# Optimization experiments

Measured on AMD Instinct MI355X. Metric: run time of the kernel, lower is better.

## Reference

```python
import jax, jax.numpy as jnp
import numpy as np

DIM = 256
STATE = 128
RANK = 64
BATCH = 16
H = 64
W = 64
BLOCK = 64
LN_EPS = 1e-5


def _linear(z, w, b):
    # torch nn.Linear: z @ w.T + b, w: [out, in]
    return jnp.matmul(z, w.T) + b


def _depthwise_conv1d(y, conv_w, conv_b):
    # y: [B, L, D] -> torch Conv1d(D, D, k=7, pad=3, groups=D)
    lhs = jnp.transpose(y, (0, 2, 1))  # [B, D, L]
    out = jax.lax.conv_general_dilated(
        lhs, conv_w, window_strides=(1,), padding=[(3, 3)],
        feature_group_count=STATE,
        dimension_numbers=("NCH", "OIH", "NCH"))
    out = out + conv_b[None, :, None]
    return jnp.transpose(out, (0, 2, 1))  # [B, L, D]


def _scan_parallel(seq, in_proj_w, in_proj_b, U, V, B_w, B_b, out_w, out_b,
                   conv_w, conv_b):
    # seq: [B, L, C]; L > PARALLEL_THRESHOLD path of the torch module
    Bn, L, _ = seq.shape
    x = _linear(seq, in_proj_w, in_proj_b)   # [B, L, D]
    bx = _linear(x, B_w, B_b)                # [B, L, D]
    n_blocks = (L + BLOCK - 1) // BLOCK
    pad_len = n_blocks * BLOCK - L
    if pad_len > 0:
        bx = jnp.pad(bx, ((0, 0), (0, pad_len), (0, 0)))
    # [B, n_blocks, BLOCK, D] -> scan over time axis BLOCK
    bx_blocks = bx.reshape(Bn, n_blocks, BLOCK, STATE)
    bx_t = jnp.transpose(bx_blocks, (2, 0, 1, 3))  # [BLOCK, B, n_blocks, D]

    def step(h, xt):
        # h: [B, n_blocks, D]; low-rank transition h @ V @ U^T + Bx
        h = jnp.matmul(jnp.matmul(h, V), U.T) + xt
        return h, h

    h0 = jnp.zeros((Bn, n_blocks, STATE), dtype=seq.dtype)
    _, ys = jax.lax.scan(step, h0, bx_t)           # [BLOCK, B, n_blocks, D]
    y_flat = jnp.transpose(ys, (1, 2, 0, 3)).reshape(Bn, n_blocks * BLOCK, STATE)
    y_flat = y_flat + _depthwise_conv1d(y_flat, conv_w, conv_b)
    if pad_len > 0:
        y_flat = y_flat[:, :L, :]
    return _linear(y_flat, out_w, out_b)           # [B, L, C]


def _layer_norm(z, g, b):
    mu = jnp.mean(z, axis=-1, keepdims=True)
    var = jnp.var(z, axis=-1, keepdims=True)
    return (z - mu) * jax.lax.rsqrt(var + LN_EPS) * g + b


def setup_inputs() -> dict:
    key = jax.random.key(0)
    ks = jax.random.split(key, 16)
    s = 0.02
    return {
        "x": jax.random.normal(ks[0], (BATCH, DIM, H, W), dtype=jnp.float32),
        "in_proj_w": jax.random.normal(ks[1], (STATE, DIM)) * s,
        "in_proj_b": jnp.zeros((STATE,), jnp.float32),
        "U": jax.random.normal(ks[2], (STATE, RANK)) * s,
        "V": jax.random.normal(ks[3], (STATE, RANK)) * s,
        "B_w": jax.random.normal(ks[4], (STATE, STATE)) * s,
        "B_b": jnp.zeros((STATE,), jnp.float32),
        "out_w": jax.random.normal(ks[5], (DIM, STATE)) * s,
        "out_b": jnp.zeros((DIM,), jnp.float32),
        "gate_w": jax.random.normal(ks[6], (DIM, DIM)) * s,
        "gate_b": jnp.zeros((DIM,), jnp.float32),
        "norm_g": jnp.ones((DIM,), jnp.float32),
        "norm_b": jnp.zeros((DIM,), jnp.float32),
        "conv_w": jax.random.normal(ks[7], (STATE, 1, 7)) * s,
        "conv_b": jnp.zeros((STATE,), jnp.float32),
    }


def reference(x, in_proj_w, in_proj_b, U, V, B_w, B_b, out_w, out_b,
              gate_w, gate_b, norm_g, norm_b, conv_w, conv_b):
    Bn, C, h, w = x.shape
    seq_lr = jnp.transpose(x, (0, 2, 3, 1)).reshape(Bn, h * w, C)
    seq_rl = seq_lr[:, ::-1, :]
    scan = lambda s: _scan_parallel(s, in_proj_w, in_proj_b, U, V, B_w, B_b,
                                    out_w, out_b, conv_w, conv_b)
    y_lr = scan(seq_lr)
    y_rl = scan(seq_rl)[:, ::-1, :]
    y = 0.5 * (y_lr + y_rl)
    gate = jax.nn.sigmoid(_linear(seq_lr, gate_w, gate_b))
    y = gate * y
    y = _layer_norm(y + seq_lr, norm_g, norm_b)
    y = jnp.transpose(y.reshape(Bn, h, w, C), (0, 3, 1, 2))
    state_seq = _linear(seq_lr, in_proj_w, in_proj_b)
    return y, state_seq
```

## Files before the change

### kernel.cpp

```cpp
#include <hip/hip_runtime.h>
#include <hip/hip_bf16.h>

#define DIMC 256
#define STATE 128
#define RANK 64
#define NBATCH 16
#define LSEQ 4096
#define NROWS (NBATCH*LSEQ)
#define LN_EPS 1e-5f
#define XSTR 264
#define X1STR 136

typedef __attribute__((ext_vector_type(8))) short frag8;
typedef __attribute__((ext_vector_type(4))) float f32x4;

union AFrag { __hip_bfloat16 h[8]; frag8 f; };
union Pack4 { __hip_bfloat16 h[4]; uint2 u; };
union Pack8 { __hip_bfloat16 h[8]; uint4 u; };

__device__ inline void gload_lds16(const void* g, void* l) {
    __builtin_amdgcn_global_load_lds((const __attribute__((address_space(1))) void*)g,
                                     (__attribute__((address_space(3))) void*)l, 16, 0, 0);
}

__device__ inline void stage_wslice(const __hip_bfloat16* __restrict__ W, int Krow, int k0,
                                    __hip_bfloat16* dst, int t, int nrows) {
    const int lane = t & 63, w = t >> 6;
    const int rounds = nrows >> 6;
    for (int j = 0; j < rounds; ++j) {
        int base = (w*rounds + j) << 10;
        int X = base + lane*16;
        int r = X >> 6;
        int cg = (X >> 4) & 3;
        const __hip_bfloat16* src = W + (size_t)r*Krow + k0 + ((cg ^ ((r>>1)&3)) << 3);
        gload_lds16(src, (char*)dst + base);
    }
}
__device__ inline frag8 ld_wfrag(const __hip_bfloat16* buf, int row, int q) {
    return *(const frag8*)((const char*)buf + (row<<6) + ((q ^ ((row>>1)&3))<<4));
}

__global__ __launch_bounds__(128) void a_kernel(const float* __restrict__ U, const float* __restrict__ V,
                                                __hip_bfloat16* __restrict__ At) {
    int i = blockIdx.x, j = threadIdx.x;
    float s = 0.f;
    #pragma unroll
    for (int r = 0; r < RANK; ++r) s += V[i*RANK + r] * U[j*RANK + r];
    At[j*STATE + i] = __float2bfloat16(s);
}

__global__ __launch_bounds__(256) void prep_weights(const float* __restrict__ in_w, const float* __restrict__ B_w,
                                                    const float* __restrict__ gate_w, const float* __restrict__ out_w,
                                                    __hip_bfloat16* __restrict__ in_wb, __hip_bfloat16* __restrict__ B_wb,
                                                    __hip_bfloat16* __restrict__ gate_wb, __hip_bfloat16* __restrict__ out_wb) {
    int idx = blockIdx.x*256 + threadIdx.x;
    int which = blockIdx.y;
    if (which == 0) { if (idx < STATE*DIMC)  in_wb[idx]   = __float2bfloat16(in_w[idx]); }
    else if (which == 1) { if (idx < STATE*STATE) B_wb[idx] = __float2bfloat16(B_w[idx]); }
    else if (which == 2) { if (idx < DIMC*DIMC)  gate_wb[idx] = __float2bfloat16(gate_w[idx]); }
    else { if (idx < DIMC*STATE) out_wb[idx] = __float2bfloat16(out_w[idx]); }
}

template<int LROWS>
__device__ inline void stage_x_tile(const float* __restrict__ xb, int l0,
                                    __hip_bfloat16* __restrict__ xs, int t) {
    constexpr int NP = LROWS/4;
    #pragma unroll
    for (int p = 0; p < NP; ++p) {
        int cin = (t>>2) + (p&3)*64;
        int lq  = (t&3) + (p>>2)*4;
        float4 v = *(const float4*)(xb + (size_t)cin*LSEQ + l0 + lq*4);
        int lb = lq*4;
        xs[(size_t)(lb+0)*XSTR + (cin ^ 0 )] = __float2bfloat16(v.x);
        xs[(size_t)(lb+1)*XSTR + (cin ^ 8 )] = __float2bfloat16(v.y);
        xs[(size_t)(lb+2)*XSTR + (cin ^ 16)] = __float2bfloat16(v.z);
        xs[(size_t)(lb+3)*XSTR + (cin ^ 24)] = __float2bfloat16(v.w);
    }
}
__device__ inline frag8 ld_xfrag(const __hip_bfloat16* __restrict__ xs, int row, int k) {
    return *(const frag8*)(xs + (size_t)row*XSTR + (k ^ ((row&3)<<3)));
}

__global__ __launch_bounds__(256) void gemm_inB(const float* __restrict__ x,
                                                const __hip_bfloat16* __restrict__ in_wb, const float* __restrict__ in_b,
                                                const __hip_bfloat16* __restrict__ B_wb, const float* __restrict__ B_b,
                                                float* __restrict__ state_out, float* __restrict__ bx) {
    __shared__ __hip_bfloat16 xs[64*XSTR];
    __shared__ __hip_bfloat16 wsl[2][4096];
    __hip_bfloat16* x1s = xs;
    const int t = threadIdx.x;
    const int lane = t & 63;
    const int c = lane & 15, q = lane >> 4;
    const int wm = t >> 6;
    const int r0 = blockIdx.x * 64;
    const int b = r0 >> 12, l0 = r0 & 4095;

    stage_x_tile<64>(x + (size_t)b*DIMC*LSEQ, l0, xs, t);
    stage_wslice(in_wb, DIMC, 0, wsl[0], t, STATE);
    __syncthreads();

    f32x4 acc[8] = {};
    #pragma unroll
    for (int i = 0; i < 8; ++i) {
        if (i < 7) stage_wslice(in_wb, DIMC, (i+1)*32, wsl[(i+1)&1], t, STATE);
        frag8 af = ld_xfrag(xs, wm*16 + c, i*32 + q*8);
        #pragma unroll
        for (int nt = 0; nt < 8; ++nt) {
            frag8 bf = ld_wfrag(wsl[i&1], nt*16 + c, q);
            acc[nt] = __builtin_amdgcn_mfma_f32_16x16x32_bf16(af, bf, acc[nt], 0, 0, 0);
        }
        __syncthreads();
    }

    stage_wslice(B_wb, STATE, 0, wsl[0], t, STATE);

    #pragma unroll
    for (int nt = 0; nt < 8; ++nt) {
        float bb = in_b[nt*16 + c];
        int col = nt*16 + c;
        #pragma unroll
        for (int r = 0; r < 4; ++r) {
            int row = wm*16 + q*4 + r;
            float v = acc[nt][r] + bb;
            state_out[(size_t)(r0 + row)*STATE + col] = v;
            x1s[(size_t)row*X1STR + (col ^ ((row&3)<<3))] = __float2bfloat16(v);
        }
    }
    __syncthreads();

    f32x4 acc2[8] = {};
    #pragma unroll
    for (int i = 0; i < 4; ++i) {
        if (i < 3) stage_wslice(B_wb, STATE, (i+1)*32, wsl[(i+1)&1], t, STATE);
        int row = wm*16 + c;
        frag8 af = *(const frag8*)(x1s + (size_t)row*X1STR + (((i*32) + q*8) ^ ((row&3)<<3)));
        #pragma unroll
        for (int nt = 0; nt < 8; ++nt) {
            frag8 bf = ld_wfrag(wsl[i&1], nt*16 + c, q);
            acc2[nt] = __builtin_amdgcn_mfma_f32_16x16x32_bf16(af, bf, acc2[nt], 0, 0, 0);
        }
        __syncthreads();
    }
    const int orow = r0 + wm*16 + q*4;
    #pragma unroll
    for (int nt = 0; nt < 8; ++nt) {
        float bb = B_b[nt*16 + c];
        #pragma unroll
        for (int r = 0; r < 4; ++r)
            bx[(size_t)(orow + r)*STATE + nt*16 + c] = acc2[nt][r] + bb;
    }
}

#define HSTRIDE 144
__global__ __launch_bounds__(256, 1) void scan_mfma(const float* __restrict__ bx,
                                                    const __hip_bfloat16* __restrict__ At,
                                                    __hip_bfloat16* __restrict__ ylr,
                                                    __hip_bfloat16* __restrict__ yrl) {
    __shared__ __hip_bfloat16 Hb[16 * HSTRIDE];
    const int t = threadIdx.x;
    const int l = t & 63;
    const int wm = t >> 6;
    const int c = l & 15;
    const int q = l >> 4;

    const int S   = blockIdx.x * 16 + c;
    const int dir = S >> 10;
    const int b   = (S >> 6) & 15;
    const int blk = S & 63;
    const int lp0 = blk * 64;
    const int lorig0 = dir ? (LSEQ - 1 - lp0) : lp0;
    const int sgnstep = dir ? -STATE : STATE;

    const float* bxrow = bx + ((size_t)b*LSEQ + lorig0)*STATE;
    __hip_bfloat16* yrow = (dir ? yrl : ylr) + ((size_t)b*LSEQ + lp0)*STATE;

    frag8 afr[2][4];
    #pragma unroll
    for (int mm = 0; mm < 2; ++mm)
        #pragma unroll
        for (int kc = 0; kc < 4; ++kc)
            afr[mm][kc] = *(const frag8*)(At + (size_t)((wm*2+mm)*16 + c)*STATE + kc*32 + q*8);

    for (int k = t; k < 16*HSTRIDE; k += 256) Hb[k] = __float2bfloat16(0.f);
    __syncthreads();

    f32x4 pf[2];
    #pragma unroll
    for (int mm = 0; mm < 2; ++mm)
        pf[mm] = *(const f32x4*)(bxrow + (wm*2+mm)*16 + q*4);

    for (int tt = 0; tt < 64; ++tt) {
        frag8 bfr[4];
        #pragma unroll
        for (int kc = 0; kc < 4; ++kc)
            bfr[kc] = *(const frag8*)(&Hb[c*HSTRIDE + kc*32 + q*8]);

        f32x4 acc[2];
        #pragma unroll
        for (int mm = 0; mm < 2; ++mm) {
            f32x4 a = {0.f, 0.f, 0.f, 0.f};
            #pragma unroll
            for (int kc = 0; kc < 4; ++kc)
                a = __builtin_amdgcn_mfma_f32_16x16x32_bf16(afr[mm][kc], bfr[kc], a, 0, 0, 0);
            acc[mm] = a + pf[mm];
        }
        if (tt < 63) {
            bxrow += sgnstep;
            #pragma unroll
            for (int mm = 0; mm < 2; ++mm)
                pf[mm] = *(const f32x4*)(bxrow + (wm*2+mm)*16 + q*4);
        }

        Pack4 pk[2];
        #pragma unroll
        for (int mm = 0; mm < 2; ++mm) {
            pk[mm].h[0] = __float2bfloat16(acc[mm][0]);
            pk[mm].h[1] = __float2bfloat16(acc[mm][1]);
            pk[mm].h[2] = __float2bfloat16(acc[mm][2]);
            pk[mm].h[3] = __float2bfloat16(acc[mm][3]);
        }
        #pragma unroll
        for (int mm = 0; mm < 2; ++mm)
            *(uint2*)(yrow + (wm*2+mm)*16 + q*4) = pk[mm].u;
        yrow += STATE;

        __syncthreads();
        #pragma unroll
        for (int mm = 0; mm < 2; ++mm)
            *(uint2*)(&Hb[c*HSTRIDE + (wm*2+mm)*16 + q*4]) = pk[mm].u;
        __syncthreads();
    }
}

__global__ __launch_bounds__(128) void conv_combine(const __hip_bfloat16* __restrict__ ylr,
                                                    const __hip_bfloat16* __restrict__ yrl,
                                                    const float* __restrict__ conv_w, const float* __restrict__ conv_b,
                                                    __hip_bfloat16* __restrict__ u) {
    const int t = threadIdx.x;
    const int s8 = (t & 15) * 8;
    const int l = blockIdx.x * 8 + (t >> 4);
    const int b = blockIdx.y;

    float wv[8][7];
    #pragma unroll
    for (int j = 0; j < 8; ++j)
        #pragma unroll
        for (int i = 0; i < 7; ++i) wv[j][i] = conv_w[(s8+j)*7 + i];

    const __hip_bfloat16* plr = ylr + (size_t)b*LSEQ*STATE;
    const __hip_bfloat16* prl = yrl + (size_t)b*LSEQ*STATE;

    float acc[8];
    {
        Pack8 v; v.u = *(const uint4*)(plr + (size_t)l*STATE + s8);
        #pragma unroll
        for (int j = 0; j < 8; ++j) acc[j] = __bfloat162float(v.h[j]);
    }
    #pragma unroll
    for (int i = 0; i < 7; ++i) {
        int qq = l - 3 + i;
        if (qq >= 0 && qq < LSEQ) {
            Pack8 v; v.u = *(const uint4*)(plr + (size_t)qq*STATE + s8);
            #pragma unroll
            for (int j = 0; j < 8; ++j) acc[j] += wv[j][i] * __bfloat162float(v.h[j]);
        }
    }
    const int lp = LSEQ - 1 - l;
    {
        Pack8 v; v.u = *(const uint4*)(prl + (size_t)lp*STATE + s8);
        #pragma unroll
        for (int j = 0; j < 8; ++j) acc[j] += __bfloat162float(v.h[j]);
    }
    #pragma unroll
    for (int i = 0; i < 7; ++i) {
        int qq = lp - 3 + i;
        if (qq >= 0 && qq < LSEQ) {
            Pack8 v; v.u = *(const uint4*)(prl + (size_t)qq*STATE + s8);
            #pragma unroll
            for (int j = 0; j < 8; ++j) acc[j] += wv[j][i] * __bfloat162float(v.h[j]);
        }
    }
    Pack8 o;
    #pragma unroll
    for (int j = 0; j < 8; ++j) o.h[j] = __float2bfloat16(0.5f*acc[j] + conv_b[s8+j]);
    *(uint4*)(u + ((size_t)b*LSEQ + l)*STATE + s8) = o.u;
}

__global__ __launch_bounds__(256) void fused_out(const float* __restrict__ x, const __hip_bfloat16* __restrict__ ub,
    const __hip_bfloat16* __restrict__ out_wb, const float* __restrict__ out_b,
    const __hip_bfloat16* __restrict__ gate_wb, const float* __restrict__ gate_b,
    const float* __restrict__ norm_g, const float* __restrict__ norm_b,
    float* __restrict__ y) {
    __shared__ __hip_bfloat16 xs[32*XSTR];
    __shared__ __hip_bfloat16 wsl[2][8192];
    __shared__ float lnbuf[2][2][16][2];
    const int t = threadIdx.x;
    const int lane = t & 63, c = lane & 15, q = lane >> 4;
    const int w = t >> 6, wm = w >> 1, wc = w & 1;
    const int r0 = blockIdx.x * 32;
    const int b = r0 >> 12, l0 = r0 & 4095;

    stage_x_tile<32>(x + (size_t)b*DIMC*LSEQ, l0, xs, t);
    frag8 ufr[4];
    {
        const int arow = r0 + wm*16 + c;
        #pragma unroll
        for (int kc = 0; kc < 4; ++kc)
            ufr[kc] = *(const frag8*)(ub + (size_t)arow*STATE + kc*32 + q*8);
    }
    stage_wslice(gate_wb, DIMC, 0, wsl[0], t, DIMC);
    __syncthreads();

    f32x4 accg[8] = {};
    f32x4 acco[8] = {};
    #pragma unroll
    for (int i = 0; i < 12; ++i) {
        if (i < 11) {
            if (i < 7) stage_wslice(gate_wb, DIMC, (i+1)*32, wsl[(i+1)&1], t, DIMC);
            else       stage_wslice(out_wb,  STATE, (i-7)*32, wsl[(i+1)&1], t, DIMC);
        }
        if (i < 8) {
            frag8 af = ld_xfrag(xs, wm*16 + c, i*32 + q*8);
            #pragma unroll
            for (int nt = 0; nt < 8; ++nt) {
                frag8 bf = ld_wfrag(wsl[i&1], wc*128 + nt*16 + c, q);
                accg[nt] = __builtin_amdgcn_mfma_f32_16x16x32_bf16(af, bf, accg[nt], 0, 0, 0);
            }
        } else {
            frag8 af = ufr[i-8];
            #pragma unroll
            for (int nt = 0; nt < 8; ++nt) {
                frag8 bf = ld_wfrag(wsl[i&1], wc*128 + nt*16 + c, q);
                acco[nt] = __builtin_amdgcn_mfma_f32_16x16x32_bf16(af, bf, acco[nt], 0, 0, 0);
            }
        }
        __syncthreads();
    }

    float s1[4] = {0.f,0.f,0.f,0.f}, s2[4] = {0.f,0.f,0.f,0.f};
    #pragma unroll
    for (int nt = 0; nt < 8; ++nt) {
        int col = wc*128 + nt*16 + c;
        float gb = gate_b[col], ob = out_b[col];
        #pragma unroll
        for (int r = 0; r < 4; ++r) {
            int row = wm*16 + q*4 + r;
            float res = __bfloat162float(xs[(size_t)row*XSTR + (col ^ ((row&3)<<3))]);
            float g = 1.f/(1.f + expf(-(accg[nt][r] + gb)));
            float v = g*(acco[nt][r] + ob) + res;
            accg[nt][r] = v;
            s1[r] += v; s2[r] += v*v;
        }
    }
    #pragma unroll
    for (int m = 1; m <= 8; m <<= 1) {
        #pragma unroll
        for (int r = 0; r < 4; ++r) {
            s1[r] += __shfl_xor(s1[r], m);
            s2[r] += __shfl_xor(s2[r], m);
        }
    }
    if (c == 0) {
        #pragma unroll
        for (int r = 0; r < 4; ++r) {
            lnbuf[wm][wc][q*4 + r][0] = s1[r];
            lnbuf[wm][wc][q*4 + r][1] = s2[r];
        }
    }
    __syncthreads();
    float mu[4], rstd[4];
    #pragma unroll
    for (int r = 0; r < 4; ++r) {
        int row16 = q*4 + r;
        float t1 = lnbuf[wm][0][row16][0] + lnbuf[wm][1][row16][0];
        float t2 = lnbuf[wm][0][row16][1] + lnbuf[wm][1][row16][1];
        float m_ = t1 * (1.f/256.f);
        mu[r] = m_;
        rstd[r] = rsqrtf(t2 * (1.f/256.f) - m_*m_ + LN_EPS);
    }
    #pragma unroll
    for (int nt = 0; nt < 8; ++nt) {
        int col = wc*128 + nt*16 + c;
        float g = norm_g[col], be = norm_b[col];
        float4 v4;
        v4.x = (accg[nt][0] - mu[0]) * rstd[0] * g + be;
        v4.y = (accg[nt][1] - mu[1]) * rstd[1] * g + be;
        v4.z = (accg[nt][2] - mu[2]) * rstd[2] * g + be;
        v4.w = (accg[nt][3] - mu[3]) * rstd[3] * g + be;
        *(float4*)(y + ((size_t)b*DIMC + col)*LSEQ + l0 + wm*16 + q*4) = v4;
    }
}

extern "C" void kernel_launch(void* const* d_in, const int* in_sizes, int n_in,
                              void* d_out, int out_size, void* d_ws, size_t ws_size,
                              hipStream_t stream) {
    const float* x      = (const float*)d_in[0];
    const float* in_w   = (const float*)d_in[1];
    const float* in_b   = (const float*)d_in[2];
    const float* U      = (const float*)d_in[3];
    const float* V      = (const float*)d_in[4];
    const float* B_w    = (const float*)d_in[5];
    const float* B_b    = (const float*)d_in[6];
    const float* out_w  = (const float*)d_in[7];
    const float* out_b  = (const float*)d_in[8];
    const float* gate_w = (const float*)d_in[9];
    const float* gate_b = (const float*)d_in[10];
    const float* norm_g = (const float*)d_in[11];
    const float* norm_b = (const float*)d_in[12];
    const float* conv_w = (const float*)d_in[13];
    const float* conv_b = (const float*)d_in[14];

    float* yfinal = (float*)d_out;
    float* state_out = yfinal + (size_t)NBATCH*DIMC*LSEQ;

    float* ws  = (float*)d_ws;
    float* bxu = ws;
    __hip_bfloat16* ub = (__hip_bfloat16*)ws;
    __hip_bfloat16* Atb16  = (__hip_bfloat16*)(ws + (size_t)NROWS*STATE);
    __hip_bfloat16* in_wb  = Atb16 + STATE*STATE;
    __hip_bfloat16* B_wb   = in_wb + STATE*DIMC;
    __hip_bfloat16* gate_wb= B_wb + STATE*STATE;
    __hip_bfloat16* out_wb = gate_wb + DIMC*DIMC;

    __hip_bfloat16* ylr = (__hip_bfloat16*)yfinal;
    __hip_bfloat16* yrl = ylr + (size_t)NROWS*STATE;

    a_kernel<<<dim3(STATE), dim3(STATE), 0, stream>>>(U, V, Atb16);
    prep_weights<<<dim3(256, 4), dim3(256), 0, stream>>>(in_w, B_w, gate_w, out_w,
                                                         in_wb, B_wb, gate_wb, out_wb);
    gemm_inB<<<dim3(NROWS/64), dim3(256), 0, stream>>>(x, in_wb, in_b, B_wb, B_b, state_out, bxu);
    scan_mfma<<<dim3(128), dim3(256), 0, stream>>>(bxu, Atb16, ylr, yrl);
    conv_combine<<<dim3(LSEQ/8, NBATCH), dim3(128), 0, stream>>>(ylr, yrl, conv_w, conv_b, ub);
    fused_out<<<dim3(NROWS/32), dim3(256), 0, stream>>>(x, ub, out_wb, out_b, gate_wb, gate_b,
                                                        norm_g, norm_b, yfinal);
    (void)in_sizes; (void)n_in; (void)out_size; (void)ws_size;
}
```

Baseline: 158.1 us.

## Use 512-thread blocks with 2-way column split and vectorized x-tile staging

The input and output GEMM kernels now run with 512 threads (8 waves). In gemm_inB each wave computes half the output columns, and fused_out handles 64 rows per block instead of 32, so each staged weight slice is reused across more rows. The x tile transpose is rewritten to read four channels per thread and write packed 4-element bf16 vectors with an XOR swizzle, replacing scalar LDS stores. This is meant to raise wave-level parallelism and cut LDS store and weight-staging traffic per row, at the cost of larger shared-memory use per block and possibly lower occupancy.

```diff
diff --git a/kernel.cpp b/kernel.cpp
--- a/kernel.cpp
+++ b/kernel.cpp
@@ -14,7 +14,6 @@
 typedef __attribute__((ext_vector_type(8))) short frag8;
 typedef __attribute__((ext_vector_type(4))) float f32x4;
 
-union AFrag { __hip_bfloat16 h[8]; frag8 f; };
 union Pack4 { __hip_bfloat16 h[4]; uint2 u; };
 union Pack8 { __hip_bfloat16 h[8]; uint4 u; };
 
@@ -23,12 +22,14 @@
                                      (__attribute__((address_space(3))) void*)l, 16, 0, 0);
 }
 
+template<int NROWSW, int NTHR>
 __device__ inline void stage_wslice(const __hip_bfloat16* __restrict__ W, int Krow, int k0,
-                                    __hip_bfloat16* dst, int t, int nrows) {
+                                    __hip_bfloat16* dst, int t) {
+    constexpr int ROUNDS = (NROWSW*64) / (NTHR*16);
     const int lane = t & 63, w = t >> 6;
-    const int rounds = nrows >> 6;
-    for (int j = 0; j < rounds; ++j) {
-        int base = (w*rounds + j) << 10;
+    #pragma unroll
+    for (int j = 0; j < ROUNDS; ++j) {
+        int base = (w*ROUNDS + j) << 10;
         int X = base + lane*16;
         int r = X >> 6;
         int cg = (X >> 4) & 3;
@@ -61,27 +62,39 @@
     else { if (idx < DIMC*STATE) out_wb[idx] = __float2bfloat16(out_w[idx]); }
 }
 
-template<int LROWS>
-__device__ inline void stage_x_tile(const float* __restrict__ xb, int l0,
-                                    __hip_bfloat16* __restrict__ xs, int t) {
-    constexpr int NP = LROWS/4;
-    #pragma unroll
-    for (int p = 0; p < NP; ++p) {
-        int cin = (t>>2) + (p&3)*64;
-        int lq  = (t&3) + (p>>2)*4;
-        float4 v = *(const float4*)(xb + (size_t)cin*LSEQ + l0 + lq*4);
-        int lb = lq*4;
-        xs[(size_t)(lb+0)*XSTR + (cin ^ 0 )] = __float2bfloat16(v.x);
-        xs[(size_t)(lb+1)*XSTR + (cin ^ 8 )] = __float2bfloat16(v.y);
-        xs[(size_t)(lb+2)*XSTR + (cin ^ 16)] = __float2bfloat16(v.z);
-        xs[(size_t)(lb+3)*XSTR + (cin ^ 24)] = __float2bfloat16(v.w);
+template<int NTHR>
+__device__ inline void stage_x64(const float* __restrict__ xb, int l0,
+                                 __hip_bfloat16* __restrict__ xs, int t) {
+    constexpr int UN = 1024 / NTHR;
+    #pragma unroll
+    for (int uu = 0; uu < UN; ++uu) {
+        int unit = t + uu*NTHR;
+        int lg = unit & 15, cg = unit >> 4;
+        int l = lg*4;
+        float4 v0 = *(const float4*)(xb + (size_t)(cg*4+0)*LSEQ + l0 + l);
+        float4 v1 = *(const float4*)(xb + (size_t)(cg*4+1)*LSEQ + l0 + l);
+        float4 v2 = *(const float4*)(xb + (size_t)(cg*4+2)*LSEQ + l0 + l);
+        float4 v3 = *(const float4*)(xb + (size_t)(cg*4+3)*LSEQ + l0 + l);
+        const float* p0 = (const float*)&v0; const float* p1 = (const float*)&v1;
+        const float* p2 = (const float*)&v2; const float* p3 = (const float*)&v3;
+        #pragma unroll
+        for (int li = 0; li < 4; ++li) {
+            Pack4 p;
+            p.h[0] = __float2bfloat16(p0[li]);
+            p.h[1] = __float2bfloat16(p1[li]);
+            p.h[2] = __float2bfloat16(p2[li]);
+            p.h[3] = __float2bfloat16(p3[li]);
+            int row = l + li;
+            int col = (cg*4) ^ ((row&3)<<3);
+            *(uint2*)(xs + (size_t)row*XSTR + col) = p.u;
+        }
     }
 }
 __device__ inline frag8 ld_xfrag(const __hip_bfloat16* __restrict__ xs, int row, int k) {
     return *(const frag8*)(xs + (size_t)row*XSTR + (k ^ ((row&3)<<3)));
 }
 
-__global__ __launch_bounds__(256) void gemm_inB(const float* __restrict__ x,
+__global__ __launch_bounds__(512) void gemm_inB(const float* __restrict__ x,
                                                 const __hip_bfloat16* __restrict__ in_wb, const float* __restrict__ in_b,
                                                 const __hip_bfloat16* __restrict__ B_wb, const float* __restrict__ B_b,
                                                 float* __restrict__ state_out, float* __restrict__ bx) {
@@ -91,33 +104,33 @@
     const int t = threadIdx.x;
     const int lane = t & 63;
     const int c = lane & 15, q = lane >> 4;
-    const int wm = t >> 6;
+    const int w = t >> 6, wm = w >> 1, wc = w & 1;
     const int r0 = blockIdx.x * 64;
     const int b = r0 >> 12, l0 = r0 & 4095;
 
-    stage_x_tile<64>(x + (size_t)b*DIMC*LSEQ, l0, xs, t);
-    stage_wslice(in_wb, DIMC, 0, wsl[0], t, STATE);
+    stage_x64<512>(x + (size_t)b*DIMC*LSEQ, l0, xs, t);
+    stage_wslice<STATE,512>(in_wb, DIMC, 0, wsl[0], t);
     __syncthreads();
 
-    f32x4 acc[8] = {};
+    f32x4 acc[4] = {};
     #pragma unroll
     for (int i = 0; i < 8; ++i) {
-        if (i < 7) stage_wslice(in_wb, DIMC, (i+1)*32, wsl[(i+1)&1], t, STATE);
+        if (i < 7) stage_wslice<STATE,512>(in_wb, DIMC, (i+1)*32, wsl[(i+1)&1], t);
         frag8 af = ld_xfrag(xs, wm*16 + c, i*32 + q*8);
         #pragma unroll
-        for (int nt = 0; nt < 8; ++nt) {
-            frag8 bf = ld_wfrag(wsl[i&1], nt*16 + c, q);
+        for (int nt = 0; nt < 4; ++nt) {
+            frag8 bf = ld_wfrag(wsl[i&1], wc*64 + nt*16 + c, q);
             acc[nt] = __builtin_amdgcn_mfma_f32_16x16x32_bf16(af, bf, acc[nt], 0, 0, 0);
         }
         __syncthreads();
     }
 
-    stage_wslice(B_wb, STATE, 0, wsl[0], t, STATE);
-
-    #pragma unroll
-    for (int nt = 0; nt < 8; ++nt) {
-        float bb = in_b[nt*16 + c];
-        int col = nt*16 + c;
+    stage_wslice<STATE,512>(B_wb, STATE, 0, wsl[0], t);
+
+    #pragma unroll
+    for (int nt = 0; nt < 4; ++nt) {
+        int col = wc*64 + nt*16 + c;
+        float bb = in_b[col];
         #pragma unroll
         for (int r = 0; r < 4; ++r) {
             int row = wm*16 + q*4 + r;
@@ -128,26 +141,27 @@
     }
     __syncthreads();
 
-    f32x4 acc2[8] = {};
+    f32x4 acc2[4] = {};
     #pragma unroll
     for (int i = 0; i < 4; ++i) {
-        if (i < 3) stage_wslice(B_wb, STATE, (i+1)*32, wsl[(i+1)&1], t, STATE);
+        if (i < 3) stage_wslice<STATE,512>(B_wb, STATE, (i+1)*32, wsl[(i+1)&1], t);
         int row = wm*16 + c;
         frag8 af = *(const frag8*)(x1s + (size_t)row*X1STR + (((i*32) + q*8) ^ ((row&3)<<3)));
         #pragma unroll
-        for (int nt = 0; nt < 8; ++nt) {
-            frag8 bf = ld_wfrag(wsl[i&1], nt*16 + c, q);
+        for (int nt = 0; nt < 4; ++nt) {
+            frag8 bf = ld_wfrag(wsl[i&1], wc*64 + nt*16 + c, q);
             acc2[nt] = __builtin_amdgcn_mfma_f32_16x16x32_bf16(af, bf, acc2[nt], 0, 0, 0);
         }
         __syncthreads();
     }
     const int orow = r0 + wm*16 + q*4;
     #pragma unroll
-    for (int nt = 0; nt < 8; ++nt) {
-        float bb = B_b[nt*16 + c];
+    for (int nt = 0; nt < 4; ++nt) {
+        int col = wc*64 + nt*16 + c;
+        float bb = B_b[col];
         #pragma unroll
         for (int r = 0; r < 4; ++r)
-            bx[(size_t)(orow + r)*STATE + nt*16 + c] = acc2[nt][r] + bb;
+            bx[(size_t)(orow + r)*STATE + col] = acc2[nt][r] + bb;
     }
 }
 
@@ -286,21 +300,21 @@
     *(uint4*)(u + ((size_t)b*LSEQ + l)*STATE + s8) = o.u;
 }
 
-__global__ __launch_bounds__(256) void fused_out(const float* __restrict__ x, const __hip_bfloat16* __restrict__ ub,
+__global__ __launch_bounds__(512) void fused_out(const float* __restrict__ x, const __hip_bfloat16* __restrict__ ub,
     const __hip_bfloat16* __restrict__ out_wb, const float* __restrict__ out_b,
     const __hip_bfloat16* __restrict__ gate_wb, const float* __restrict__ gate_b,
     const float* __restrict__ norm_g, const float* __restrict__ norm_b,
     float* __restrict__ y) {
-    __shared__ __hip_bfloat16 xs[32*XSTR];
+    __shared__ __hip_bfloat16 xs[64*XSTR];
     __shared__ __hip_bfloat16 wsl[2][8192];
-    __shared__ float lnbuf[2][2][16][2];
+    __shared__ float lnbuf[4][2][16][2];
     const int t = threadIdx.x;
     const int lane = t & 63, c = lane & 15, q = lane >> 4;
     const int w = t >> 6, wm = w >> 1, wc = w & 1;
-    const int r0 = blockIdx.x * 32;
+    const int r0 = blockIdx.x * 64;
     const int b = r0 >> 12, l0 = r0 & 4095;
 
-    stage_x_tile<32>(x + (size_t)b*DIMC*LSEQ, l0, xs, t);
+    stage_x64<512>(x + (size_t)b*DIMC*LSEQ, l0, xs, t);
     frag8 ufr[4];
     {
         const int arow = r0 + wm*16 + c;
@@ -308,7 +322,7 @@
         for (int kc = 0; kc < 4; ++kc)
             ufr[kc] = *(const frag8*)(ub + (size_t)arow*STATE + kc*32 + q*8);
     }
-    stage_wslice(gate_wb, DIMC, 0, wsl[0], t, DIMC);
+    stage_wslice<DIMC,512>(gate_wb, DIMC, 0, wsl[0], t);
     __syncthreads();
 
     f32x4 accg[8] = {};
@@ -316,8 +330,8 @@
     #pragma unroll
     for (int i = 0; i < 12; ++i) {
         if (i < 11) {
-            if (i < 7) stage_wslice(gate_wb, DIMC, (i+1)*32, wsl[(i+1)&1], t, DIMC);
-            else       stage_wslice(out_wb,  STATE, (i-7)*32, wsl[(i+1)&1], t, DIMC);
+            if (i < 7) stage_wslice<DIMC,512>(gate_wb, DIMC, (i+1)*32, wsl[(i+1)&1], t);
+            else       stage_wslice<DIMC,512>(out_wb,  STATE, (i-7)*32, wsl[(i+1)&1], t);
         }
         if (i < 8) {
             frag8 af = ld_xfrag(xs, wm*16 + c, i*32 + q*8);
@@ -428,10 +442,10 @@
     a_kernel<<<dim3(STATE), dim3(STATE), 0, stream>>>(U, V, Atb16);
     prep_weights<<<dim3(256, 4), dim3(256), 0, stream>>>(in_w, B_w, gate_w, out_w,
                                                          in_wb, B_wb, gate_wb, out_wb);
-    gemm_inB<<<dim3(NROWS/64), dim3(256), 0, stream>>>(x, in_wb, in_b, B_wb, B_b, state_out, bxu);
+    gemm_inB<<<dim3(NROWS/64), dim3(512), 0, stream>>>(x, in_wb, in_b, B_wb, B_b, state_out, bxu);
     scan_mfma<<<dim3(128), dim3(256), 0, stream>>>(bxu, Atb16, ylr, yrl);
     conv_combine<<<dim3(LSEQ/8, NBATCH), dim3(128), 0, stream>>>(ylr, yrl, conv_w, conv_b, ub);
-    fused_out<<<dim3(NROWS/32), dim3(256), 0, stream>>>(x, ub, out_wb, out_b, gate_wb, gate_b,
+    fused_out<<<dim3(NROWS/64), dim3(512), 0, stream>>>(x, ub, out_wb, out_b, gate_wb, gate_b,
                                                         norm_g, norm_b, yfinal);
     (void)in_sizes; (void)n_in; (void)out_size; (void)ws_size;
 }
```

After: 150.8 us, median of 3. -4.6%, faster.
